# Performance work log

Measured on AMD Instinct MI355X. Metric: run time of the kernel, lower is better.

## Reference

```python
import jax, jax.numpy as jnp
import numpy as np

B, T, C, H = 2, 2048, 1024, 16
D = C // H  # head dim = 64


def setup_inputs() -> dict:
    key = jax.random.key(0)
    ks = jax.random.split(key, 5)
    s_in = 1.0 / np.sqrt(C)
    return {
        "x": jax.random.normal(ks[0], (B, T, C), dtype=jnp.float32),
        "W_qkv": jax.random.uniform(ks[1], (C, 3 * C), jnp.float32, -s_in, s_in),
        "b_qkv": jax.random.uniform(ks[2], (3 * C,), jnp.float32, -s_in, s_in),
        "W_proj": jax.random.uniform(ks[3], (C, C), jnp.float32, -s_in, s_in),
        "b_proj": jax.random.uniform(ks[4], (C,), jnp.float32, -s_in, s_in),
    }


def reference(x, W_qkv, b_qkv, W_proj, b_proj):
    Bx, Tx, Cx = x.shape
    qkv = x @ W_qkv + b_qkv                      # [B,T,3C]
    q, k, v = jnp.split(qkv, 3, axis=2)          # each [B,T,C]
    # [B,T,C] -> [B,H,T,D]
    q = q.reshape(Bx, Tx, H, D).transpose(0, 2, 1, 3)
    k = k.reshape(Bx, Tx, H, D).transpose(0, 2, 1, 3)
    v = v.reshape(Bx, Tx, H, D).transpose(0, 2, 1, 3)
    scale = 1.0 / jnp.sqrt(jnp.asarray(D, dtype=x.dtype))
    scores = jnp.einsum("bhqd,bhkd->bhqk", q, k) * scale  # [B,H,T,T]
    causal = jnp.tril(jnp.ones((Tx, Tx), dtype=bool))
    scores = jnp.where(causal, scores, jnp.finfo(x.dtype).min)
    attn = jax.nn.softmax(scores, axis=-1)
    y = jnp.einsum("bhqk,bhkd->bhqd", attn, v)   # [B,H,T,D]
    y = y.transpose(0, 2, 1, 3).reshape(Bx, Tx, Cx)
    return y @ W_proj + b_proj
```

## Files before the change

kernel.cpp:

```cpp
#include <hip/hip_runtime.h>
#include <hip/hip_bf16.h>

#define Bb 2
#define Tt 2048
#define Cc 1024
#define Hh 16
#define Dd 64

typedef __bf16 bf16x8 __attribute__((ext_vector_type(8)));
typedef __bf16 bf16x4 __attribute__((ext_vector_type(4)));
typedef float f32x4 __attribute__((ext_vector_type(4)));

#define MFMA16(a, b, c) __builtin_amdgcn_mfma_f32_16x16x32_bf16((a), (b), (c), 0, 0, 0)

__device__ __forceinline__ bf16x8 ldg8(const __hip_bfloat16* p) {
  return *reinterpret_cast<const bf16x8*>(p);
}
__device__ __forceinline__ bf16x8 lds8(const __bf16* p) {
  return *reinterpret_cast<const bf16x8*>(p);
}

__device__ __forceinline__ void load_lds16(const __hip_bfloat16* g, __hip_bfloat16* l) {
  __builtin_amdgcn_global_load_lds(
      (const __attribute__((address_space(1))) void*)g,
      (__attribute__((address_space(3))) void*)l, 16, 0, 0);
}

__global__ __launch_bounds__(256) void cvt_f32_bf16(
    const float* __restrict__ in, __hip_bfloat16* __restrict__ out, int n) {
  const int i = (blockIdx.x * 256 + threadIdx.x) * 4;
  if (i + 3 < n) {
    const float4 v = *reinterpret_cast<const float4*>(in + i);
    out[i + 0] = __float2bfloat16(v.x);
    out[i + 1] = __float2bfloat16(v.y);
    out[i + 2] = __float2bfloat16(v.z);
    out[i + 3] = __float2bfloat16(v.w);
  }
}

__global__ __launch_bounds__(256) void transpose_cvt(
    const float* __restrict__ in, __hip_bfloat16* __restrict__ out,
    int R, int Cn) {
  __shared__ float tile[32][33];
  const int c0 = blockIdx.x * 32, r0 = blockIdx.y * 32;
  const int tx = threadIdx.x, ty = threadIdx.y;
#pragma unroll
  for (int i = 0; i < 32; i += 8)
    tile[ty + i][tx] = in[(size_t)(r0 + ty + i) * Cn + c0 + tx];
  __syncthreads();
#pragma unroll
  for (int i = 0; i < 32; i += 8)
    out[(size_t)(c0 + ty + i) * R + r0 + tx] = __float2bfloat16(tile[tx][ty + i]);
}

__global__ __launch_bounds__(256) void qkv_gemm(
    const __hip_bfloat16* __restrict__ x, const __hip_bfloat16* __restrict__ WT,
    const float* __restrict__ bias,
    __hip_bfloat16* __restrict__ Q, __hip_bfloat16* __restrict__ Kd,
    __hip_bfloat16* __restrict__ VT) {
  __shared__ __hip_bfloat16 As[128 * 32];
  __shared__ __hip_bfloat16 Bs[128 * 32];
  const int tid = threadIdx.x;
  const int wave = tid >> 6, lane = tid & 63;
  const int l16 = lane & 15, quad = lane >> 4;
  const int m0 = blockIdx.y * 128, n0 = blockIdx.x * 128;
  const int wm = (wave >> 1) * 64, wn = (wave & 1) * 64;

  const int srow = wave * 32 + (lane >> 2);
  const int kseg = (lane & 3) * 8;

  f32x4 acc[4][4] = {};

  for (int k0 = 0; k0 < Cc; k0 += 32) {
    __syncthreads();
#pragma unroll
    for (int j = 0; j < 2; ++j) {
      load_lds16(x + (size_t)(m0 + srow + j * 16) * Cc + k0 + kseg,
                 As + (wave * 32 + j * 16) * 32);
      load_lds16(WT + (size_t)(n0 + srow + j * 16) * Cc + k0 + kseg,
                 Bs + (wave * 32 + j * 16) * 32);
    }
    __syncthreads();

    bf16x8 af[4], bfr[4];
#pragma unroll
    for (int i = 0; i < 4; ++i) {
      af[i] = ldg8(As + (wm + i * 16 + l16) * 32 + quad * 8);
      bfr[i] = ldg8(Bs + (wn + i * 16 + l16) * 32 + quad * 8);
    }
#pragma unroll
    for (int i = 0; i < 4; ++i)
#pragma unroll
      for (int jn = 0; jn < 4; ++jn)
        acc[i][jn] = MFMA16(af[i], bfr[jn], acc[i][jn]);
  }

  const int sect = n0 >> 10;
#pragma unroll
  for (int jn = 0; jn < 4; ++jn) {
    const int n = n0 + wn + jn * 16 + l16;
    const float bv = bias[n];
    const int ch = n & 1023;
    const int h = ch >> 6, d = ch & 63;
#pragma unroll
    for (int i = 0; i < 4; ++i) {
#pragma unroll
      for (int r = 0; r < 4; ++r) {
        const int m = m0 + wm + i * 16 + quad * 4 + r;
        const int b = m >> 11, t = m & 2047;
        const __hip_bfloat16 o = __float2bfloat16(acc[i][jn][r] + bv);
        const int bh = b * Hh + h;
        if (sect == 0)      Q[((size_t)bh * Tt + t) * Dd + d] = o;
        else if (sect == 1) Kd[((size_t)bh * Tt + t) * Dd + d] = o;
        else                VT[((size_t)bh * Dd + d) * Tt + t] = o;
      }
    }
  }
}

__global__ __launch_bounds__(256, 2) void attn(
    const __hip_bfloat16* __restrict__ Q, const __hip_bfloat16* __restrict__ K,
    const __hip_bfloat16* __restrict__ VT, __hip_bfloat16* __restrict__ O) {
  const int tid = threadIdx.x;
  const int wave = tid >> 6, lane = tid & 63;
  const int l16 = lane & 15, quad = lane >> 4;
  const int bh = blockIdx.z * Hh + blockIdx.y;

  const __hip_bfloat16* Qh = Q + (size_t)bh * Tt * Dd;
  const __hip_bfloat16* Kh = K + (size_t)bh * Tt * Dd;
  const __hip_bfloat16* Vh = VT + (size_t)bh * Dd * Tt;
  __hip_bfloat16* Oh = O + (size_t)bh * Tt * Dd;

  __shared__ __align__(16) __bf16 Kt[64 * 72];
  __shared__ __align__(16) __bf16 Vt[64 * 72];
  __shared__ __align__(16) __bf16 Pt[4][2][16 * 72];

  const float SC = 0.18033688011112042f;
  const int skey = tid >> 3, sd = (tid & 7) * 8;

  const int qbA = blockIdx.x;
  const int qbB = (Tt / 64 - 1) - qbA;
  const int qrowA = qbA * 64 + wave * 16 + l16;
  const int qrowB = qbB * 64 + wave * 16 + l16;

  const bf16x8 qA0 = ldg8(Qh + (size_t)qrowA * Dd + quad * 8);
  const bf16x8 qA1 = ldg8(Qh + (size_t)qrowA * Dd + 32 + quad * 8);
  const bf16x8 qB0 = ldg8(Qh + (size_t)qrowB * Dd + quad * 8);
  const bf16x8 qB1 = ldg8(Qh + (size_t)qrowB * Dd + 32 + quad * 8);

  f32x4 oA[4] = {}, oB[4] = {};
  float lA = 0.f, lB = 0.f;

  const int nkB = qbB + 1;

  bf16x8 ka = ldg8(Kh + (size_t)skey * Dd + sd);
  bf16x8 kb = ldg8(Kh + (size_t)(32 + skey) * Dd + sd);
  bf16x8 va = ldg8(Vh + (size_t)skey * Tt + sd);
  bf16x8 vb = ldg8(Vh + (size_t)(32 + skey) * Tt + sd);

  for (int kt0 = 0; kt0 < nkB; ++kt0) {
    const int k0 = kt0 * 64;
    __syncthreads();
    *reinterpret_cast<bf16x8*>(&Kt[skey * 72 + sd]) = ka;
    *reinterpret_cast<bf16x8*>(&Kt[(32 + skey) * 72 + sd]) = kb;
    *reinterpret_cast<bf16x8*>(&Vt[skey * 72 + sd]) = va;
    *reinterpret_cast<bf16x8*>(&Vt[(32 + skey) * 72 + sd]) = vb;
    if (kt0 + 1 < nkB) {
      const int k1 = k0 + 64;
      ka = ldg8(Kh + (size_t)(k1 + skey) * Dd + sd);
      kb = ldg8(Kh + (size_t)(k1 + 32 + skey) * Dd + sd);
      va = ldg8(Vh + (size_t)skey * Tt + k1 + sd);
      vb = ldg8(Vh + (size_t)(32 + skey) * Tt + k1 + sd);
    }
    __syncthreads();

    const bool doA = (kt0 <= qbA);
    const bool diagB = (kt0 == qbB), diagA = (kt0 == qbA);

    f32x4 stB[4], stA[4];
#pragma unroll
    for (int kt = 0; kt < 4; ++kt) {
      const __bf16* kr = &Kt[(kt * 16 + l16) * 72 + quad * 8];
      const bf16x8 k0f = lds8(kr), k1f = lds8(kr + 32);
      f32x4 zb = {};
      zb = MFMA16(k0f, qB0, zb);
      stB[kt] = MFMA16(k1f, qB1, zb);
      if (doA) {
        f32x4 za = {};
        za = MFMA16(k0f, qA0, za);
        stA[kt] = MFMA16(k1f, qA1, za);
      }
    }

#pragma unroll
    for (int kt = 0; kt < 4; ++kt) {
      bf16x4 pk;
#pragma unroll
      for (int r = 0; r < 4; ++r) {
        float p = exp2f(stB[kt][r] * SC);
        if (diagB) {
          const int key = k0 + kt * 16 + quad * 4 + r;
          p = (key <= qrowB) ? p : 0.f;
        }
        lB += p;
        pk[r] = (__bf16)p;
      }
      *reinterpret_cast<bf16x4*>(&Pt[wave][0][l16 * 72 + kt * 16 + quad * 4]) = pk;
    }

    if (doA) {
#pragma unroll
      for (int kt = 0; kt < 4; ++kt) {
        bf16x4 pk;
#pragma unroll
        for (int r = 0; r < 4; ++r) {
          float p = exp2f(stA[kt][r] * SC);
          if (diagA) {
            const int key = k0 + kt * 16 + quad * 4 + r;
            p = (key <= qrowA) ? p : 0.f;
          }
          lA += p;
          pk[r] = (__bf16)p;
        }
        *reinterpret_cast<bf16x4*>(&Pt[wave][1][l16 * 72 + kt * 16 + quad * 4]) = pk;
      }
    }

    const bf16x8 pB0 = lds8(&Pt[wave][0][l16 * 72 + quad * 8]);
    const bf16x8 pB1 = lds8(&Pt[wave][0][l16 * 72 + 32 + quad * 8]);
    const bf16x8 pA0 = lds8(&Pt[wave][1][l16 * 72 + quad * 8]);
    const bf16x8 pA1 = lds8(&Pt[wave][1][l16 * 72 + 32 + quad * 8]);
#pragma unroll
    for (int dt = 0; dt < 4; ++dt) {
      const __bf16* vr = &Vt[(dt * 16 + l16) * 72];
      const bf16x8 v0f = lds8(vr + quad * 8), v1f = lds8(vr + 32 + quad * 8);
      oB[dt] = MFMA16(v0f, pB0, oB[dt]);
      oB[dt] = MFMA16(v1f, pB1, oB[dt]);
      if (doA) {
        oA[dt] = MFMA16(v0f, pA0, oA[dt]);
        oA[dt] = MFMA16(v1f, pA1, oA[dt]);
      }
    }
  }

  lA += __shfl_xor(lA, 16, 64);
  lA += __shfl_xor(lA, 32, 64);
  lB += __shfl_xor(lB, 16, 64);
  lB += __shfl_xor(lB, 32, 64);

  const float invA = 1.f / lA, invB = 1.f / lB;
#pragma unroll
  for (int dt = 0; dt < 4; ++dt) {
    bf16x4 ovA, ovB;
#pragma unroll
    for (int r = 0; r < 4; ++r) {
      ovA[r] = (__bf16)(oA[dt][r] * invA);
      ovB[r] = (__bf16)(oB[dt][r] * invB);
    }
    *reinterpret_cast<bf16x4*>(&Oh[(size_t)qrowA * Dd + dt * 16 + quad * 4]) = ovA;
    *reinterpret_cast<bf16x4*>(&Oh[(size_t)qrowB * Dd + dt * 16 + quad * 4]) = ovB;
  }
}

__global__ __launch_bounds__(256) void proj_gemm(
    const __hip_bfloat16* __restrict__ O, const __hip_bfloat16* __restrict__ WT,
    const float* __restrict__ bias, float* __restrict__ out) {
  __shared__ __hip_bfloat16 As[128 * 32];
  __shared__ __hip_bfloat16 Bs[128 * 32];
  const int tid = threadIdx.x;
  const int wave = tid >> 6, lane = tid & 63;
  const int l16 = lane & 15, quad = lane >> 4;
  const int m0 = blockIdx.y * 128, n0 = blockIdx.x * 128;
  const int wm = (wave >> 1) * 64, wn = (wave & 1) * 64;

  const int srow = wave * 32 + (lane >> 2);
  const int kseg = (lane & 3) * 8;

  f32x4 acc[4][4] = {};

  for (int k0 = 0; k0 < Cc; k0 += 32) {
    const int k = k0 + kseg;
    const int h = k >> 6, d = k & 63;
    __syncthreads();
#pragma unroll
    for (int j = 0; j < 2; ++j) {
      const int m = m0 + srow + j * 16;
      const int b = m >> 11, t = m & 2047;
      load_lds16(O + ((size_t)(b * Hh + h) * Tt + t) * Dd + d,
                 As + (wave * 32 + j * 16) * 32);
      load_lds16(WT + (size_t)(n0 + srow + j * 16) * Cc + k0 + kseg,
                 Bs + (wave * 32 + j * 16) * 32);
    }
    __syncthreads();

    bf16x8 af[4], bfr[4];
#pragma unroll
    for (int i = 0; i < 4; ++i) {
      af[i] = ldg8(As + (wm + i * 16 + l16) * 32 + quad * 8);
      bfr[i] = ldg8(Bs + (wn + i * 16 + l16) * 32 + quad * 8);
    }
#pragma unroll
    for (int i = 0; i < 4; ++i)
#pragma unroll
      for (int jn = 0; jn < 4; ++jn)
        acc[i][jn] = MFMA16(af[i], bfr[jn], acc[i][jn]);
  }

#pragma unroll
  for (int jn = 0; jn < 4; ++jn) {
    const int n = n0 + wn + jn * 16 + l16;
    const float bv = bias[n];
#pragma unroll
    for (int i = 0; i < 4; ++i)
#pragma unroll
      for (int r = 0; r < 4; ++r) {
        const int m = m0 + wm + i * 16 + quad * 4 + r;
        out[(size_t)m * Cc + n] = acc[i][jn][r] + bv;
      }
  }
}

extern "C" void kernel_launch(void* const* d_in, const int* in_sizes, int n_in,
                              void* d_out, int out_size, void* d_ws, size_t ws_size,
                              hipStream_t stream) {
  const float* x      = (const float*)d_in[0];
  const float* W_qkv  = (const float*)d_in[1];
  const float* b_qkv  = (const float*)d_in[2];
  const float* W_proj = (const float*)d_in[3];
  const float* b_proj = (const float*)d_in[4];
  float* out = (float*)d_out;

  __hip_bfloat16* ws = (__hip_bfloat16*)d_ws;
  const size_t NBHTD = (size_t)Bb * Hh * Tt * Dd;
  __hip_bfloat16* Qw  = ws;
  __hip_bfloat16* Kw  = ws + NBHTD;
  __hip_bfloat16* VTw = ws + 2 * NBHTD;
  __hip_bfloat16* Ow  = ws + 3 * NBHTD;
  __hip_bfloat16* xb  = ws + 4 * NBHTD;
  __hip_bfloat16* WTqkv  = xb + NBHTD;
  __hip_bfloat16* WTproj = WTqkv + (size_t)3 * Cc * Cc;

  cvt_f32_bf16<<<dim3(4096), dim3(256), 0, stream>>>(x, xb, Bb * Tt * Cc);
  transpose_cvt<<<dim3(96, 32), dim3(32, 8), 0, stream>>>(W_qkv, WTqkv, Cc, 3 * Cc);
  transpose_cvt<<<dim3(32, 32), dim3(32, 8), 0, stream>>>(W_proj, WTproj, Cc, Cc);
  qkv_gemm<<<dim3(24, 32), 256, 0, stream>>>(xb, WTqkv, b_qkv, Qw, Kw, VTw);
  attn<<<dim3(Tt / 128, Hh, Bb), 256, 0, stream>>>(Qw, Kw, VTw, Ow);
  proj_gemm<<<dim3(8, 32), 256, 0, stream>>>(Ow, WTproj, b_proj, out);
}
```

Baseline: 194.5 us.

## Fuse x fp32-to-bf16 conversion into QKV GEMM and merge weight transposes

The standalone x conversion kernel is removed. The QKV GEMM now reads fp32 x directly, converts it in registers and writes bf16 into LDS, replacing the async global-to-LDS load for the A operand. The two weight transpose launches are merged into one kernel to save a launch. This drops an 8 MB write plus reread of x, but each GEMM block now reads fp32 x (twice the bytes) on every k-step for 24 column tiles, and the A load becomes synchronous through registers.

Result: slower. 234.0 us (+20.3%).

```diff
diff --git a/kernel.cpp b/kernel.cpp
--- a/kernel.cpp
+++ b/kernel.cpp
@@ -26,23 +26,16 @@
       (__attribute__((address_space(3))) void*)l, 16, 0, 0);
 }
 
-__global__ __launch_bounds__(256) void cvt_f32_bf16(
-    const float* __restrict__ in, __hip_bfloat16* __restrict__ out, int n) {
-  const int i = (blockIdx.x * 256 + threadIdx.x) * 4;
-  if (i + 3 < n) {
-    const float4 v = *reinterpret_cast<const float4*>(in + i);
-    out[i + 0] = __float2bfloat16(v.x);
-    out[i + 1] = __float2bfloat16(v.y);
-    out[i + 2] = __float2bfloat16(v.z);
-    out[i + 3] = __float2bfloat16(v.w);
-  }
-}
-
-__global__ __launch_bounds__(256) void transpose_cvt(
-    const float* __restrict__ in, __hip_bfloat16* __restrict__ out,
-    int R, int Cn) {
+__global__ __launch_bounds__(256) void prep_weights(
+    const float* __restrict__ Wq, const float* __restrict__ Wp,
+    __hip_bfloat16* __restrict__ WTq, __hip_bfloat16* __restrict__ WTp) {
   __shared__ float tile[32][33];
-  const int c0 = blockIdx.x * 32, r0 = blockIdx.y * 32;
+  const bool isQ = blockIdx.x < 96;
+  const float* in = isQ ? Wq : Wp;
+  __hip_bfloat16* out = isQ ? WTq : WTp;
+  const int Cn = isQ ? 3 * Cc : Cc;
+  const int c0 = (isQ ? blockIdx.x : blockIdx.x - 96) * 32;
+  const int r0 = blockIdx.y * 32;
   const int tx = threadIdx.x, ty = threadIdx.y;
 #pragma unroll
   for (int i = 0; i < 32; i += 8)
@@ -50,11 +43,11 @@
   __syncthreads();
 #pragma unroll
   for (int i = 0; i < 32; i += 8)
-    out[(size_t)(c0 + ty + i) * R + r0 + tx] = __float2bfloat16(tile[tx][ty + i]);
+    out[(size_t)(c0 + ty + i) * Cc + r0 + tx] = __float2bfloat16(tile[tx][ty + i]);
 }
 
 __global__ __launch_bounds__(256) void qkv_gemm(
-    const __hip_bfloat16* __restrict__ x, const __hip_bfloat16* __restrict__ WT,
+    const float* __restrict__ x, const __hip_bfloat16* __restrict__ WT,
     const float* __restrict__ bias,
     __hip_bfloat16* __restrict__ Q, __hip_bfloat16* __restrict__ Kd,
     __hip_bfloat16* __restrict__ VT) {
@@ -69,24 +62,41 @@
   const int srow = wave * 32 + (lane >> 2);
   const int kseg = (lane & 3) * 8;
 
+  const int arow = tid >> 1;
+  const int akseg = (tid & 1) * 16;
+
   f32x4 acc[4][4] = {};
 
   for (int k0 = 0; k0 < Cc; k0 += 32) {
     __syncthreads();
-#pragma unroll
-    for (int j = 0; j < 2; ++j) {
-      load_lds16(x + (size_t)(m0 + srow + j * 16) * Cc + k0 + kseg,
-                 As + (wave * 32 + j * 16) * 32);
+    {
+      const float* xr = x + (size_t)(m0 + arow) * Cc + k0 + akseg;
+      const f32x4 f0 = *reinterpret_cast<const f32x4*>(xr);
+      const f32x4 f1 = *reinterpret_cast<const f32x4*>(xr + 4);
+      const f32x4 f2 = *reinterpret_cast<const f32x4*>(xr + 8);
+      const f32x4 f3 = *reinterpret_cast<const f32x4*>(xr + 12);
+      bf16x8 c0, c1;
+#pragma unroll
+      for (int e = 0; e < 4; ++e) {
+        c0[e] = (__bf16)f0[e];
+        c0[4 + e] = (__bf16)f1[e];
+        c1[e] = (__bf16)f2[e];
+        c1[4 + e] = (__bf16)f3[e];
+      }
+      *reinterpret_cast<bf16x8*>(As + arow * 32 + akseg) = c0;
+      *reinterpret_cast<bf16x8*>(As + arow * 32 + akseg + 8) = c1;
+    }
+#pragma unroll
+    for (int j = 0; j < 2; ++j)
       load_lds16(WT + (size_t)(n0 + srow + j * 16) * Cc + k0 + kseg,
                  Bs + (wave * 32 + j * 16) * 32);
-    }
     __syncthreads();
 
     bf16x8 af[4], bfr[4];
 #pragma unroll
     for (int i = 0; i < 4; ++i) {
-      af[i] = ldg8(As + (wm + i * 16 + l16) * 32 + quad * 8);
-      bfr[i] = ldg8(Bs + (wn + i * 16 + l16) * 32 + quad * 8);
+      af[i] = lds8((__bf16*)As + (wm + i * 16 + l16) * 32 + quad * 8);
+      bfr[i] = lds8((__bf16*)Bs + (wn + i * 16 + l16) * 32 + quad * 8);
     }
 #pragma unroll
     for (int i = 0; i < 4; ++i)
@@ -336,14 +346,11 @@
   __hip_bfloat16* Kw  = ws + NBHTD;
   __hip_bfloat16* VTw = ws + 2 * NBHTD;
   __hip_bfloat16* Ow  = ws + 3 * NBHTD;
-  __hip_bfloat16* xb  = ws + 4 * NBHTD;
-  __hip_bfloat16* WTqkv  = xb + NBHTD;
+  __hip_bfloat16* WTqkv  = ws + 4 * NBHTD;
   __hip_bfloat16* WTproj = WTqkv + (size_t)3 * Cc * Cc;
 
-  cvt_f32_bf16<<<dim3(4096), dim3(256), 0, stream>>>(x, xb, Bb * Tt * Cc);
-  transpose_cvt<<<dim3(96, 32), dim3(32, 8), 0, stream>>>(W_qkv, WTqkv, Cc, 3 * Cc);
-  transpose_cvt<<<dim3(32, 32), dim3(32, 8), 0, stream>>>(W_proj, WTproj, Cc, Cc);
-  qkv_gemm<<<dim3(24, 32), 256, 0, stream>>>(xb, WTqkv, b_qkv, Qw, Kw, VTw);
+  prep_weights<<<dim3(128, 32), dim3(32, 8), 0, stream>>>(W_qkv, W_proj, WTqkv, WTproj);
+  qkv_gemm<<<dim3(24, 32), 256, 0, stream>>>(x, WTqkv, b_qkv, Qw, Kw, VTw);
   attn<<<dim3(Tt / 128, Hh, Bb), 256, 0, stream>>>(Qw, Kw, VTw, Ow);
   proj_gemm<<<dim3(8, 32), 256, 0, stream>>>(Ow, WTproj, b_proj, out);
 }
```
